# Kernel optimization log

Hardware: AMD Instinct MI355X
Metric: run time of the kernel (lower is better)

## Reference

```python
import jax, jax.numpy as jnp
import numpy as np
import math

B, S, D, H = 2, 2048, 1024, 16
DK = D // H

def setup_inputs() -> dict:
    key = jax.random.key(0)
    ks = jax.random.split(key, 8)
    query = jax.random.normal(ks[0], (B, S, D), dtype=jnp.float32)
    k_in = jax.random.normal(ks[1], (B, S, D), dtype=jnp.float32)
    value = jax.random.normal(ks[2], (B, S, D), dtype=jnp.float32)
    mask = jax.random.randint(ks[3], (B, S, S), 0, 2, dtype=jnp.int32)
    scale = 1.0 / math.sqrt(D)
    Wq = jax.random.normal(ks[4], (D, D), dtype=jnp.float32) * scale
    Wk = jax.random.normal(ks[5], (D, D), dtype=jnp.float32) * scale
    Wv = jax.random.normal(ks[6], (D, D), dtype=jnp.float32) * scale
    Wo = jax.random.normal(ks[7], (D, D), dtype=jnp.float32) * scale
    return {"query": query, "key": k_in, "value": value, "mask": mask,
            "Wq": Wq, "Wk": Wk, "Wv": Wv, "Wo": Wo}

def reference(query, key, value, mask, Wq, Wk, Wv, Wo):
    # torch Linear(no bias): y = x @ W.T ; weights are [out, in]
    def split_heads(x):  # [B,S,D] -> [B,H,S,DK]
        return x.reshape(B, S, H, DK).transpose(0, 2, 1, 3)
    q = split_heads(query @ Wq.T)
    k = split_heads(key @ Wk.T)
    v = split_heads(value @ Wv.T)
    scores = jnp.einsum('bhqd,bhkd->bhqk', q, k) / jnp.sqrt(jnp.float32(DK))
    scores = jnp.where(mask[:, None, :, :] == 0, jnp.float32(-1e9), scores)
    p_attn = jax.nn.softmax(scores, axis=-1)  # dropout is identity in eval mode
    attn = jnp.einsum('bhqk,bhkd->bhqd', p_attn, v)
    out = attn.transpose(0, 2, 1, 3).reshape(B, S, D)
    return out @ Wo.T
```

## Files before the change

### kernel.cpp

```cpp
#include <hip/hip_runtime.h>
#include <hip/hip_bf16.h>
#include <cstdint>
#include <cstddef>

constexpr int BATCH = 2;
constexpr int SEQ   = 2048;
constexpr int DIM   = 1024;
constexpr int NH    = 16;
constexpr int DK    = 64;

typedef unsigned short u16;
typedef unsigned int   u32;
typedef unsigned long long u64;

typedef __attribute__((ext_vector_type(8))) short bf16x8;
typedef __attribute__((ext_vector_type(8))) unsigned short u16x8;
typedef __attribute__((ext_vector_type(4))) float f32x4;
typedef __attribute__((ext_vector_type(16))) float f32x16;
typedef __attribute__((ext_vector_type(4))) unsigned int u32x4;

__device__ __forceinline__ u16 f2bf(float f) {
  u32 u = __builtin_bit_cast(u32, f);
  u32 r = (u + 0x7FFFu + ((u >> 16) & 1u)) >> 16;
  return (u16)r;
}

__device__ __forceinline__ u32 pack_bf2(float a, float b) {
  __hip_bfloat162 h2 = __float22bfloat162_rn(make_float2(a, b));
  u32 r;
  __builtin_memcpy(&r, &h2, 4);
  return r;
}

__device__ __forceinline__ float fexp2(float x) {
#if __has_builtin(__builtin_amdgcn_exp2f)
  return __builtin_amdgcn_exp2f(x);
#else
  return exp2f(x);
#endif
}

__device__ __forceinline__ u32 bit_to_allones(u32 word, int bit) {
#if __has_builtin(__builtin_amdgcn_sbfe)
  return (u32)__builtin_amdgcn_sbfe((int)word, bit, 1);
#else
  return (u32)(((int)(word << (31 - bit))) >> 31);
#endif
}

__device__ __forceinline__ void plswap32(u32& a, u32& b) {
  asm volatile("v_permlane32_swap_b32 %0, %1" : "+v"(a), "+v"(b));
}

__device__ __forceinline__ void gload16(const u16* g, u16* l) {
  __builtin_amdgcn_global_load_lds(
      (const __attribute__((address_space(1))) void*)g,
      (__attribute__((address_space(3))) void*)l, 16, 0, 0);
}

constexpr size_t QS  = (size_t)BATCH * SEQ * DIM;
constexpr size_t WSZ = (size_t)DIM * DIM;
constexpr int CVT_BLOCKS  = (int)((3 * QS + 4 * WSZ) / (256 * 8));
constexpr int MASK_BLOCKS = (BATCH * SEQ * SEQ) / 256;

__global__ __launch_bounds__(256) void prep(const float* __restrict__ q,
                                            const float* __restrict__ k,
                                            const float* __restrict__ v,
                                            const float* __restrict__ wq,
                                            const float* __restrict__ wk,
                                            const float* __restrict__ wv,
                                            const float* __restrict__ wo,
                                            u16* __restrict__ dst,
                                            const int* __restrict__ mask,
                                            u64* __restrict__ bits) {
  const int bid = blockIdx.x;
  if (bid < CVT_BLOCKS) {
    const size_t i = ((size_t)bid * 256 + threadIdx.x) * 8;
    const float* s;
    if      (i < QS)              s = q  + i;
    else if (i < 2 * QS)          s = k  + (i - QS);
    else if (i < 3 * QS)          s = v  + (i - 2 * QS);
    else if (i < 3 * QS + WSZ)     s = wq + (i - 3 * QS);
    else if (i < 3 * QS + 2 * WSZ) s = wk + (i - 3 * QS - WSZ);
    else if (i < 3 * QS + 3 * WSZ) s = wv + (i - 3 * QS - 2 * WSZ);
    else                           s = wo + (i - 3 * QS - 3 * WSZ);
    f32x4 a = *(const f32x4*)s, b2 = *(const f32x4*)(s + 4);
    u32x4 t;
    t[0] = pack_bf2(a[0], a[1]);  t[1] = pack_bf2(a[2], a[3]);
    t[2] = pack_bf2(b2[0], b2[1]); t[3] = pack_bf2(b2[2], b2[3]);
    *(u16x8*)(dst + i) = __builtin_bit_cast(u16x8, t);
  } else {
    const int gt = (bid - CVT_BLOCKS) * 256 + threadIdx.x;
    u64 m = __ballot(mask[gt] != 0);
    if ((threadIdx.x & 63) == 0) bits[gt >> 6] = m;
  }
}

__global__ __launch_bounds__(256) void transpose_v(const u16* __restrict__ V,
                                                   u16* __restrict__ Vt) {
  __shared__ u16 t[64][68];
  const int st = blockIdx.x * 64;
  const int bh = blockIdx.y;
  const int b = bh >> 4, h = bh & 15;
  const int tid = threadIdx.x;
#pragma unroll
  for (int s = 0; s < 2; ++s) {
    int c = tid + s * 256;
    int row = c >> 3, c8 = c & 7;
    u16x8 vv = *(const u16x8*)(V + ((size_t)(b * SEQ + st + row)) * DIM + h * DK + c8 * 8);
#pragma unroll
    for (int j = 0; j < 8; ++j) t[row][c8 * 8 + j] = vv[j];
  }
  __syncthreads();
#pragma unroll
  for (int s = 0; s < 2; ++s) {
    int c = tid + s * 256;
    int dk = c >> 3, sc = c & 7;
    u16x8 ov;
#pragma unroll
    for (int j = 0; j < 8; ++j) ov[j] = t[sc * 8 + j][dk];
    *(u16x8*)(Vt + ((size_t)bh * DK + dk) * SEQ + st + sc * 8) = ov;
  }
}

struct GemmParams {
  const void* A[3];
  const void* B[3];
  void*       C[3];
  float       alpha[3];
};

template <bool OUTF32>
__global__ __launch_bounds__(256) void gemm_nt(GemmParams p, int M, int N, int K) {
  const int z = blockIdx.z;
  __shared__ __align__(16) u16 As[128 * 64];
  __shared__ __align__(16) u16 Bs[128 * 64];

  const int nbx = gridDim.x, nby = gridDim.y;
  const int lid = blockIdx.y * nbx + blockIdx.x;
  const int xcd = lid & 7, idx = lid >> 3;
  const int rows_per_xcd = nby >> 3;
  const int by = xcd * rows_per_xcd + idx / nbx;
  const int bx = idx % nbx;

  const int tid = threadIdx.x;
  const int lane = tid & 63, w = tid >> 6;
  const int l31 = lane & 31, hi = lane >> 5;
  const int bm = by * 128, bn = bx * 128;
  const int wm = (w >> 1) * 64, wn = (w & 1) * 64;

  const u16* A = (const u16*)p.A[z];
  const u16* B = (const u16*)p.B[z];

  const int srow = lane >> 3;
  const int gchk = (lane & 7) ^ srow;

  f32x16 acc[2][2] = {};

  for (int k0 = 0; k0 < K; k0 += 64) {
#pragma unroll
    for (int j = 0; j < 4; ++j) {
      const int row = 32 * w + 8 * j + srow;
      gload16(&A[(size_t)(bm + row) * K + k0 + gchk * 8], &As[2048 * w + 512 * j]);
      gload16(&B[(size_t)(bn + row) * K + k0 + gchk * 8], &Bs[2048 * w + 512 * j]);
    }
    __syncthreads();

#pragma unroll
    for (int ks = 0; ks < 4; ++ks) {
      bf16x8 af[2], bf[2];
#pragma unroll
      for (int mb = 0; mb < 2; ++mb) {
        const int row = wm + mb * 32 + l31;
        af[mb] = *(const bf16x8*)&As[row * 64 + ((2 * ks + hi) ^ (row & 7)) * 8];
      }
#pragma unroll
      for (int nb = 0; nb < 2; ++nb) {
        const int row = wn + nb * 32 + l31;
        bf[nb] = *(const bf16x8*)&Bs[row * 64 + ((2 * ks + hi) ^ (row & 7)) * 8];
      }
      __builtin_amdgcn_s_setprio(1);
#pragma unroll
      for (int mb = 0; mb < 2; ++mb)
#pragma unroll
        for (int nb = 0; nb < 2; ++nb)
          acc[mb][nb] = __builtin_amdgcn_mfma_f32_32x32x16_bf16(af[mb], bf[nb], acc[mb][nb], 0, 0, 0);
      __builtin_amdgcn_s_setprio(0);
    }
    __syncthreads();
  }

  const float alpha = p.alpha[z];
#pragma unroll
  for (int mb = 0; mb < 2; ++mb)
#pragma unroll
    for (int nb = 0; nb < 2; ++nb)
#pragma unroll
      for (int r = 0; r < 16; ++r) {
        const int row = bm + wm + mb * 32 + (r & 3) + 8 * (r >> 2) + 4 * hi;
        const int col = bn + wn + nb * 32 + l31;
        float val = acc[mb][nb][r] * alpha;
        if (OUTF32) ((float*)p.C[z])[(size_t)row * N + col] = val;
        else        ((u16*)p.C[z])[(size_t)row * N + col]  = f2bf(val);
      }
}

__global__ __launch_bounds__(512, 8) void attn_fwd(const u16* __restrict__ Qb,
                                                   const u16* __restrict__ Kb,
                                                   const u16* __restrict__ Vtb,
                                                   const u64* __restrict__ mbits,
                                                   u16* __restrict__ Ob) {
  const int h = blockIdx.y, b = blockIdx.z;
  const int tid = threadIdx.x;
  const int lane = tid & 63, w = tid >> 6;
  const int l31 = lane & 31, hi = lane >> 5;
  const int half = w >> 2, wq = w & 3;

  __shared__ __align__(16) u16 Kbuf[2][8192];
  __shared__ __align__(16) u16 Vbuf[8192];
  __shared__ float Lsh[4][64];

  const int q0 = blockIdx.x * 128 + wq * 32;
  const int rsw = l31 & 7;

  bf16x8 qreg[4];
  {
    const u16* qp = Qb + ((size_t)(b * SEQ + q0 + l31)) * DIM + h * DK + 8 * hi;
#pragma unroll
    for (int s = 0; s < 4; ++s) qreg[s] = *(const bf16x8*)(qp + 16 * s);
  }

  const int grow = (w << 3) + (lane >> 3);
  const int gchk = (lane & 7) ^ (grow & 7);
  const u16* kbase  = Kb + ((size_t)b * SEQ + grow) * DIM + h * DK + gchk * 8;
  const u16* vtbase = Vtb + ((size_t)(b * NH + h) * DK + grow) * SEQ + gchk * 8;
  const u64* mrow   = mbits + (size_t)(b * SEQ + q0 + l31) * (SEQ / 64) + half * 16;

  f32x16 o[2] = {};
  float lsum = 0.f;

  gload16(kbase,                      &Kbuf[0][0]    + w * 512);
  gload16(kbase + (size_t)1024 * DIM, &Kbuf[0][4096] + w * 512);
  u64 mbc = mrow[0];
  __syncthreads();

  for (int kt = 0; kt < 16; ++kt) {
    const int cur = kt & 1;

    gload16(vtbase + kt * 64,                      &Vbuf[0]    + w * 512);
    gload16(vtbase + 1024 + kt * 64,               &Vbuf[4096] + w * 512);
    u64 mbn = mbc;
    if (kt < 15) {
      const u16* ks = kbase + (size_t)(kt + 1) * 64 * DIM;
      gload16(ks,                       &Kbuf[cur ^ 1][0]    + w * 512);
      gload16(ks + (size_t)1024 * DIM,  &Kbuf[cur ^ 1][4096] + w * 512);
      mbn = mrow[kt + 1];
    }
    const u16* const Kc = &Kbuf[cur][half * 4096];
    const u16* const Vc = &Vbuf[half * 4096];

    const u64 nmb = ~mbc;
    const u64 mbh = nmb >> (hi * 4);
    const u32 nm[2] = {(u32)mbh, (u32)(mbh >> 32)};
    f32x16 sc[2];
#pragma unroll
    for (int kb = 0; kb < 2; ++kb)
#pragma unroll
      for (int r = 0; r < 16; ++r) {
        const int key = (r & 3) + 8 * (r >> 2);
        u32 t = bit_to_allones(nm[kb], key) & 0xC6EA6000u;
        sc[kb][r] = __builtin_bit_cast(float, t);
      }

#pragma unroll
    for (int kb = 0; kb < 2; ++kb) {
      const int row = kb * 32 + l31;
#pragma unroll
      for (int s = 0; s < 4; ++s) {
        bf16x8 kf = *(const bf16x8*)&Kc[row * 64 + ((2 * s + hi) ^ rsw) * 8];
        sc[kb] = __builtin_amdgcn_mfma_f32_32x32x16_bf16(kf, qreg[s], sc[kb], 0, 0, 0);
      }
    }

#pragma unroll
    for (int kb = 0; kb < 2; ++kb)
#pragma unroll
      for (int r = 0; r < 16; ++r)
        sc[kb][r] = fexp2(sc[kb][r]);
    float s8[8];
#pragma unroll
    for (int i = 0; i < 8; ++i)
      s8[i] = (sc[0][i] + sc[0][i + 8]) + (sc[1][i] + sc[1][i + 8]);
    lsum += ((s8[0] + s8[1]) + (s8[2] + s8[3])) + ((s8[4] + s8[5]) + (s8[6] + s8[7]));

    bf16x8 pa[2][2];
#pragma unroll
    for (int kb = 0; kb < 2; ++kb) {
      u32 wv[8];
#pragma unroll
      for (int t = 0; t < 8; ++t)
        wv[t] = pack_bf2(sc[kb][2 * t], sc[kb][2 * t + 1]);
      plswap32(wv[0], wv[2]);
      plswap32(wv[1], wv[3]);
      plswap32(wv[4], wv[6]);
      plswap32(wv[5], wv[7]);
      u32x4 f0 = {wv[0], wv[1], wv[2], wv[3]};
      u32x4 f1 = {wv[4], wv[5], wv[6], wv[7]};
      pa[kb][0] = __builtin_bit_cast(bf16x8, f0);
      pa[kb][1] = __builtin_bit_cast(bf16x8, f1);
    }

    __syncthreads();

#pragma unroll
    for (int kb = 0; kb < 2; ++kb)
#pragma unroll
      for (int ks = 0; ks < 2; ++ks) {
        bf16x8 pf = pa[kb][ks];
#pragma unroll
        for (int d = 0; d < 2; ++d) {
          const int row = l31 + 32 * d;
          bf16x8 vf = *(const bf16x8*)&Vc[row * 64 + ((4 * kb + 2 * ks + hi) ^ rsw) * 8];
          o[d] = __builtin_amdgcn_mfma_f32_32x32x16_bf16(pf, vf, o[d], 0, 0, 0);
        }
      }
    mbc = mbn;
    __syncthreads();
  }

  lsum += __shfl_xor(lsum, 32, 64);
  f32x4* const oa4 = (f32x4*)&Kbuf[0][0];
  if (half == 1) {
    f32x4* dst = oa4 + (size_t)(wq * 64 + lane) * 8;
#pragma unroll
    for (int d = 0; d < 2; ++d)
#pragma unroll
      for (int cc = 0; cc < 4; ++cc) {
        f32x4 t = {o[d][cc * 4 + 0], o[d][cc * 4 + 1], o[d][cc * 4 + 2], o[d][cc * 4 + 3]};
        dst[(d * 4 + cc) ^ (lane & 7)] = t;
      }
    Lsh[wq][lane] = lsum;
  }
  __syncthreads();
  if (half == 0) {
    const float ltot = lsum + Lsh[wq][lane];
    const float linv = 1.0f / ltot;
    const f32x4* src = oa4 + (size_t)(wq * 64 + lane) * 8;
    f32x4 ov[8];
#pragma unroll
    for (int c = 0; c < 8; ++c) ov[c] = src[c ^ (lane & 7)];
    float lr[16];
#pragma unroll
    for (int r = 0; r < 16; ++r)
      lr[r] = __shfl(linv, (r & 3) + 8 * (r >> 2) + 4 * hi, 64);
#pragma unroll
    for (int d = 0; d < 2; ++d)
#pragma unroll
      for (int r = 0; r < 16; ++r) {
        const float om = o[d][r] + ov[d * 4 + (r >> 2)][r & 3];
        const int qloc = (r & 3) + 8 * (r >> 2) + 4 * hi;
        Ob[(size_t)(b * SEQ + q0 + qloc) * DIM + h * DK + l31 + 32 * d] = f2bf(om * lr[r]);
      }
  }
}

extern "C" void kernel_launch(void* const* d_in, const int* in_sizes, int n_in,
                              void* d_out, int out_size, void* d_ws, size_t ws_size,
                              hipStream_t stream) {
  const float* q    = (const float*)d_in[0];
  const float* k    = (const float*)d_in[1];
  const float* v    = (const float*)d_in[2];
  const int*   mask = (const int*)d_in[3];
  const float* Wq   = (const float*)d_in[4];
  const float* Wk   = (const float*)d_in[5];
  const float* Wv   = (const float*)d_in[6];
  const float* Wo   = (const float*)d_in[7];
  float* out = (float*)d_out;

  char* ws = (char*)d_ws;
  u64* mbits = (u64*)ws;
  u16* XB  = (u16*)(ws + 0x0100000);
  u16* xq = XB, *xk = XB + QS, *xv = XB + 2 * QS;
  u16* wqb = XB + 3 * QS, *wkb = wqb + WSZ, *wvb = wkb + WSZ, *wob = wvb + WSZ;
  u16* Qb  = (u16*)(ws + 0x2100000);
  u16* Kb  = (u16*)(ws + 0x2900000);
  u16* Vb  = (u16*)(ws + 0x3100000);
  u16* Vtb = (u16*)(ws + 0x3900000);
  u16* Ab  = (u16*)(ws + 0x4100000);

  prep<<<CVT_BLOCKS + MASK_BLOCKS, 256, 0, stream>>>(q, k, v, Wq, Wk, Wv, Wo, XB,
                                                     mask, mbits);

  GemmParams gp;
  gp.A[0] = xq;  gp.A[1] = xk;  gp.A[2] = xv;
  gp.B[0] = wqb; gp.B[1] = wkb; gp.B[2] = wvb;
  gp.C[0] = Qb;  gp.C[1] = Kb;  gp.C[2] = Vb;
  gp.alpha[0] = 0.125f * 1.44269504088896f; gp.alpha[1] = 1.0f; gp.alpha[2] = 1.0f;
  gemm_nt<false><<<dim3(DIM / 128, (BATCH * SEQ) / 128, 3), 256, 0, stream>>>(
      gp, BATCH * SEQ, DIM, DIM);

  transpose_v<<<dim3(SEQ / 64, BATCH * NH), 256, 0, stream>>>(Vb, Vtb);

  attn_fwd<<<dim3(SEQ / 128, NH, BATCH), 512, 0, stream>>>(Qb, Kb, Vtb, mbits, Ab);

  GemmParams go;
  go.A[0] = Ab; go.B[0] = wob; go.C[0] = out; go.alpha[0] = 1.0f;
  go.A[1] = go.A[2] = nullptr; go.B[1] = go.B[2] = nullptr; go.C[1] = go.C[2] = nullptr;
  go.alpha[1] = go.alpha[2] = 1.0f;
  gemm_nt<true><<<dim3(DIM / 128, (BATCH * SEQ) / 128, 1), 256, 0, stream>>>(
      go, BATCH * SEQ, DIM, DIM);
}
```

Before: 146.4 us.

## Split attention keys across four wave groups with 1024-thread blocks and double-buffered V

The attention kernel moves from 512 to 1024 threads per block. The key dimension is now split four ways instead of two, so each wave processes 32 keys per tile instead of 64. V is double-buffered alongside K, which removes the mid-iteration barrier, and the mask is read as 32-bit words. The four partial outputs are combined through shared memory in three serialized rounds with extra barriers. This raises parallelism per query tile but adds reduction cost and cuts per-wave MFMA work per barrier.

```diff
diff --git a/kernel.cpp b/kernel.cpp
--- a/kernel.cpp
+++ b/kernel.cpp
@@ -205,20 +205,20 @@
       }
 }
 
-__global__ __launch_bounds__(512, 8) void attn_fwd(const u16* __restrict__ Qb,
-                                                   const u16* __restrict__ Kb,
-                                                   const u16* __restrict__ Vtb,
-                                                   const u64* __restrict__ mbits,
-                                                   u16* __restrict__ Ob) {
+__global__ __launch_bounds__(1024, 8) void attn_fwd(const u16* __restrict__ Qb,
+                                                    const u16* __restrict__ Kb,
+                                                    const u16* __restrict__ Vtb,
+                                                    const u64* __restrict__ mbits,
+                                                    u16* __restrict__ Ob) {
   const int h = blockIdx.y, b = blockIdx.z;
   const int tid = threadIdx.x;
   const int lane = tid & 63, w = tid >> 6;
   const int l31 = lane & 31, hi = lane >> 5;
-  const int half = w >> 2, wq = w & 3;
+  const int qt = w >> 2, wq = w & 3;
 
   __shared__ __align__(16) u16 Kbuf[2][8192];
-  __shared__ __align__(16) u16 Vbuf[8192];
-  __shared__ float Lsh[4][64];
+  __shared__ __align__(16) u16 Vbuf[2][8192];
+  __shared__ float Lq[4][4][64];
 
   const int q0 = blockIdx.x * 128 + wq * 32;
   const int rsw = l31 & 7;
@@ -230,125 +230,124 @@
     for (int s = 0; s < 4; ++s) qreg[s] = *(const bf16x8*)(qp + 16 * s);
   }
 
-  const int grow = (w << 3) + (lane >> 3);
-  const int gchk = (lane & 7) ^ (grow & 7);
-  const u16* kbase  = Kb + ((size_t)b * SEQ + grow) * DIM + h * DK + gchk * 8;
-  const u16* vtbase = Vtb + ((size_t)(b * NH + h) * DK + grow) * SEQ + gchk * 8;
-  const u64* mrow   = mbits + (size_t)(b * SEQ + q0 + l31) * (SEQ / 64) + half * 16;
+  const int krow = tid >> 3;
+  const int kchk = (tid & 7) ^ (krow & 7);
+  const u16* ksrc = Kb + ((size_t)b * SEQ + (krow >> 5) * 512 + (krow & 31)) * DIM
+                       + h * DK + kchk * 8;
+  const int vrow = tid >> 4;
+  const int vg = (tid & 15) ^ (vrow & 7);
+  const u16* vsrc = Vtb + ((size_t)(b * NH + h) * DK + vrow) * SEQ
+                        + (vg >> 2) * 512 + (vg & 3) * 8;
+  const u32* mrow32 = (const u32*)mbits
+                    + (size_t)(b * SEQ + q0 + l31) * (SEQ / 32) + qt * 16;
 
   f32x16 o[2] = {};
   float lsum = 0.f;
 
-  gload16(kbase,                      &Kbuf[0][0]    + w * 512);
-  gload16(kbase + (size_t)1024 * DIM, &Kbuf[0][4096] + w * 512);
-  u64 mbc = mrow[0];
+  gload16(ksrc, &Kbuf[0][0] + w * 512);
+  gload16(vsrc, &Vbuf[0][0] + w * 512);
+  u32 mw = mrow32[0];
   __syncthreads();
 
   for (int kt = 0; kt < 16; ++kt) {
     const int cur = kt & 1;
-
-    gload16(vtbase + kt * 64,                      &Vbuf[0]    + w * 512);
-    gload16(vtbase + 1024 + kt * 64,               &Vbuf[4096] + w * 512);
-    u64 mbn = mbc;
+    u32 mwn = mw;
     if (kt < 15) {
-      const u16* ks = kbase + (size_t)(kt + 1) * 64 * DIM;
-      gload16(ks,                       &Kbuf[cur ^ 1][0]    + w * 512);
-      gload16(ks + (size_t)1024 * DIM,  &Kbuf[cur ^ 1][4096] + w * 512);
-      mbn = mrow[kt + 1];
-    }
-    const u16* const Kc = &Kbuf[cur][half * 4096];
-    const u16* const Vc = &Vbuf[half * 4096];
-
-    const u64 nmb = ~mbc;
-    const u64 mbh = nmb >> (hi * 4);
-    const u32 nm[2] = {(u32)mbh, (u32)(mbh >> 32)};
-    f32x16 sc[2];
-#pragma unroll
-    for (int kb = 0; kb < 2; ++kb)
-#pragma unroll
-      for (int r = 0; r < 16; ++r) {
-        const int key = (r & 3) + 8 * (r >> 2);
-        u32 t = bit_to_allones(nm[kb], key) & 0xC6EA6000u;
-        sc[kb][r] = __builtin_bit_cast(float, t);
+      gload16(ksrc + (size_t)(kt + 1) * 32 * DIM, &Kbuf[cur ^ 1][0] + w * 512);
+      gload16(vsrc + (kt + 1) * 32,               &Vbuf[cur ^ 1][0] + w * 512);
+      mwn = mrow32[kt + 1];
+    }
+    const u16* const Kc = &Kbuf[cur][qt * 2048];
+    const u16* const Vc = &Vbuf[cur][0];
+
+    const u32 nm = ~mw;
+    f32x16 sc;
+#pragma unroll
+    for (int r = 0; r < 16; ++r) {
+      const int bit = (r & 3) + 8 * (r >> 2) + 4 * hi;
+      u32 t = bit_to_allones(nm, bit) & 0xC6EA6000u;
+      sc[r] = __builtin_bit_cast(float, t);
+    }
+
+#pragma unroll
+    for (int s = 0; s < 4; ++s) {
+      bf16x8 kf = *(const bf16x8*)&Kc[l31 * 64 + ((2 * s + hi) ^ rsw) * 8];
+      sc = __builtin_amdgcn_mfma_f32_32x32x16_bf16(kf, qreg[s], sc, 0, 0, 0);
+    }
+
+#pragma unroll
+    for (int r = 0; r < 16; ++r)
+      sc[r] = fexp2(sc[r]);
+    float s8[8];
+#pragma unroll
+    for (int i = 0; i < 8; ++i)
+      s8[i] = sc[i] + sc[i + 8];
+    lsum += ((s8[0] + s8[1]) + (s8[2] + s8[3])) + ((s8[4] + s8[5]) + (s8[6] + s8[7]));
+
+    u32 wv[8];
+#pragma unroll
+    for (int t = 0; t < 8; ++t)
+      wv[t] = pack_bf2(sc[2 * t], sc[2 * t + 1]);
+    plswap32(wv[0], wv[2]);
+    plswap32(wv[1], wv[3]);
+    plswap32(wv[4], wv[6]);
+    plswap32(wv[5], wv[7]);
+    u32x4 f0 = {wv[0], wv[1], wv[2], wv[3]};
+    u32x4 f1 = {wv[4], wv[5], wv[6], wv[7]};
+    bf16x8 pa0 = __builtin_bit_cast(bf16x8, f0);
+    bf16x8 pa1 = __builtin_bit_cast(bf16x8, f1);
+
+#pragma unroll
+    for (int ks = 0; ks < 2; ++ks) {
+      bf16x8 pf = ks ? pa1 : pa0;
+#pragma unroll
+      for (int d = 0; d < 2; ++d) {
+        const int row = l31 + 32 * d;
+        const int g = qt * 4 + 2 * ks + hi;
+        bf16x8 vf = *(const bf16x8*)&Vc[row * 128 + (g ^ rsw) * 8];
+        o[d] = __builtin_amdgcn_mfma_f32_32x32x16_bf16(pf, vf, o[d], 0, 0, 0);
       }
-
-#pragma unroll
-    for (int kb = 0; kb < 2; ++kb) {
-      const int row = kb * 32 + l31;
-#pragma unroll
-      for (int s = 0; s < 4; ++s) {
-        bf16x8 kf = *(const bf16x8*)&Kc[row * 64 + ((2 * s + hi) ^ rsw) * 8];
-        sc[kb] = __builtin_amdgcn_mfma_f32_32x32x16_bf16(kf, qreg[s], sc[kb], 0, 0, 0);
-      }
-    }
-
-#pragma unroll
-    for (int kb = 0; kb < 2; ++kb)
-#pragma unroll
-      for (int r = 0; r < 16; ++r)
-        sc[kb][r] = fexp2(sc[kb][r]);
-    float s8[8];
-#pragma unroll
-    for (int i = 0; i < 8; ++i)
-      s8[i] = (sc[0][i] + sc[0][i + 8]) + (sc[1][i] + sc[1][i + 8]);
-    lsum += ((s8[0] + s8[1]) + (s8[2] + s8[3])) + ((s8[4] + s8[5]) + (s8[6] + s8[7]));
-
-    bf16x8 pa[2][2];
-#pragma unroll
-    for (int kb = 0; kb < 2; ++kb) {
-      u32 wv[8];
-#pragma unroll
-      for (int t = 0; t < 8; ++t)
-        wv[t] = pack_bf2(sc[kb][2 * t], sc[kb][2 * t + 1]);
-      plswap32(wv[0], wv[2]);
-      plswap32(wv[1], wv[3]);
-      plswap32(wv[4], wv[6]);
-      plswap32(wv[5], wv[7]);
-      u32x4 f0 = {wv[0], wv[1], wv[2], wv[3]};
-      u32x4 f1 = {wv[4], wv[5], wv[6], wv[7]};
-      pa[kb][0] = __builtin_bit_cast(bf16x8, f0);
-      pa[kb][1] = __builtin_bit_cast(bf16x8, f1);
-    }
-
+    }
+    mw = mwn;
     __syncthreads();
-
-#pragma unroll
-    for (int kb = 0; kb < 2; ++kb)
-#pragma unroll
-      for (int ks = 0; ks < 2; ++ks) {
-        bf16x8 pf = pa[kb][ks];
-#pragma unroll
-        for (int d = 0; d < 2; ++d) {
-          const int row = l31 + 32 * d;
-          bf16x8 vf = *(const bf16x8*)&Vc[row * 64 + ((4 * kb + 2 * ks + hi) ^ rsw) * 8];
-          o[d] = __builtin_amdgcn_mfma_f32_32x32x16_bf16(pf, vf, o[d], 0, 0, 0);
+  }
+
+  lsum += __shfl_xor(lsum, 32, 64);
+  Lq[qt][wq][lane] = lsum;
+  __syncthreads();
+
+  f32x4* const R = (f32x4*)&Kbuf[0][0];
+#pragma unroll 1
+  for (int src = 1; src < 4; ++src) {
+    if (qt == src) {
+      f32x4* dst = R + (size_t)(wq * 64 + lane) * 8;
+#pragma unroll
+      for (int d = 0; d < 2; ++d)
+#pragma unroll
+        for (int cc = 0; cc < 4; ++cc) {
+          f32x4 t = {o[d][cc * 4 + 0], o[d][cc * 4 + 1], o[d][cc * 4 + 2], o[d][cc * 4 + 3]};
+          dst[(d * 4 + cc) ^ (lane & 7)] = t;
         }
-      }
-    mbc = mbn;
+    }
     __syncthreads();
-  }
-
-  lsum += __shfl_xor(lsum, 32, 64);
-  f32x4* const oa4 = (f32x4*)&Kbuf[0][0];
-  if (half == 1) {
-    f32x4* dst = oa4 + (size_t)(wq * 64 + lane) * 8;
-#pragma unroll
-    for (int d = 0; d < 2; ++d)
-#pragma unroll
-      for (int cc = 0; cc < 4; ++cc) {
-        f32x4 t = {o[d][cc * 4 + 0], o[d][cc * 4 + 1], o[d][cc * 4 + 2], o[d][cc * 4 + 3]};
-        dst[(d * 4 + cc) ^ (lane & 7)] = t;
-      }
-    Lsh[wq][lane] = lsum;
-  }
-  __syncthreads();
-  if (half == 0) {
-    const float ltot = lsum + Lsh[wq][lane];
+    if (qt == 0) {
+      const f32x4* srcp = R + (size_t)(wq * 64 + lane) * 8;
+      f32x4 ov[8];
+#pragma unroll
+      for (int c = 0; c < 8; ++c) ov[c] = srcp[c ^ (lane & 7)];
+#pragma unroll
+      for (int d = 0; d < 2; ++d)
+#pragma unroll
+        for (int r = 0; r < 16; ++r)
+          o[d][r] += ov[d * 4 + (r >> 2)][r & 3];
+    }
+    __syncthreads();
+  }
+
+  if (qt == 0) {
+    const float ltot = Lq[0][wq][lane] + Lq[1][wq][lane]
+                     + Lq[2][wq][lane] + Lq[3][wq][lane];
     const float linv = 1.0f / ltot;
-    const f32x4* src = oa4 + (size_t)(wq * 64 + lane) * 8;
-    f32x4 ov[8];
-#pragma unroll
-    for (int c = 0; c < 8; ++c) ov[c] = src[c ^ (lane & 7)];
     float lr[16];
 #pragma unroll
     for (int r = 0; r < 16; ++r)
@@ -357,9 +356,9 @@
     for (int d = 0; d < 2; ++d)
 #pragma unroll
       for (int r = 0; r < 16; ++r) {
-        const float om = o[d][r] + ov[d * 4 + (r >> 2)][r & 3];
         const int qloc = (r & 3) + 8 * (r >> 2) + 4 * hi;
-        Ob[(size_t)(b * SEQ + q0 + qloc) * DIM + h * DK + l31 + 32 * d] = f2bf(om * lr[r]);
+        Ob[(size_t)(b * SEQ + q0 + qloc) * DIM + h * DK + l31 + 32 * d] =
+            f2bf(o[d][r] * lr[r]);
       }
   }
 }
@@ -401,7 +400,7 @@
 
   transpose_v<<<dim3(SEQ / 64, BATCH * NH), 256, 0, stream>>>(Vb, Vtb);
 
-  attn_fwd<<<dim3(SEQ / 128, NH, BATCH), 512, 0, stream>>>(Qb, Kb, Vtb, mbits, Ab);
+  attn_fwd<<<dim3(SEQ / 128, NH, BATCH), 1024, 0, stream>>>(Qb, Kb, Vtb, mbits, Ab);
 
   GemmParams go;
   go.A[0] = Ab; go.B[0] = wob; go.C[0] = out; go.alpha[0] = 1.0f;
```

Measured after the change: 359.8 us. +145.9%, slower.
